# Kernel tuning notes

Measured on AMD Instinct MI355X. Metric: run time of the kernel, lower is better.

## Reference

```python
import jax, jax.numpy as jnp
import numpy as np

LOG1000 = 6.9077542789816375  # ln(1000)


def setup_inputs() -> dict:
    key = jax.random.key(0)
    kx, kp = jax.random.split(key)
    x = jax.random.normal(kx, (65536, 128), dtype=jnp.float32)
    points = jax.random.normal(kp, (2048, 128), dtype=jnp.float32)
    beta_raw = jnp.array([-3.5], dtype=jnp.float32)
    return {"x": x, "points": points, "beta_raw": beta_raw}


def reference(x, points, beta_raw):
    t1 = jnp.sum(x * x, axis=-1, keepdims=True)            # [N, 1]
    t2 = jnp.sum(points * points, axis=-1)[None, :]        # [1, P]
    t3 = 2.0 * jnp.einsum('nd,pd->np', x, points)          # [N, P]
    d2 = jnp.clip(t1 + t2 - t3, 0.0)
    min_d = jnp.min(d2, axis=-1)                           # [N]
    # translated sigmoid
    beta = jax.nn.softplus(beta_raw)                       # [1]
    alpha = -beta * LOG1000
    return jax.nn.sigmoid((min_d + alpha) / beta)
```

## Files before the change

### kernel.cpp

```cpp
#include <hip/hip_runtime.h>


#define NROWS 65536
#define NPTS  2048
#define DIMS  128
#define LOG1000F 6.9077542789816375f
#define RPB 256
#define PPB 512
#define TPB (PPB / 16)

typedef __attribute__((ext_vector_type(8))) int i32x8;
typedef __attribute__((ext_vector_type(4))) float f32x4;

union AFrag { int d[8]; i32x8 v; };
union BFrag { uint4 u4[2]; i32x8 v; };

__global__ __launch_bounds__(256) void prep_points_kernel(
    const float* __restrict__ pts, unsigned char* __restrict__ ptsf8,
    float* __restrict__ pnorm, unsigned int* __restrict__ minws)
{
    int tid  = threadIdx.x;
    int gid  = blockIdx.x * 256 + tid;
    if (gid < NROWS) minws[gid] = 0x7F800000u;

    int lane = tid & 63;
    int w    = tid >> 6;
    int pt   = blockIdx.x * 4 + w;
    const float2 v = *reinterpret_cast<const float2*>(
        pts + (size_t)pt * DIMS + lane * 2);
    int pk = __builtin_amdgcn_cvt_pk_fp8_f32(v.x, v.y, 0, false);
    *reinterpret_cast<unsigned short*>(ptsf8 + (size_t)pt * DIMS + lane * 2) =
        (unsigned short)(pk & 0xFFFF);
    float ss = v.x * v.x + v.y * v.y;
    ss += __shfl_xor(ss, 1, 64);
    ss += __shfl_xor(ss, 2, 64);
    ss += __shfl_xor(ss, 4, 64);
    ss += __shfl_xor(ss, 8, 64);
    ss += __shfl_xor(ss, 16, 64);
    ss += __shfl_xor(ss, 32, 64);
    if (lane == 0) pnorm[pt] = ss;
}

__global__ __launch_bounds__(256, 2) void distnet_main_kernel(
    const float* __restrict__ x, const unsigned char* __restrict__ ptsf8,
    const float* __restrict__ pnorm, unsigned int* __restrict__ minws)
{
    __shared__ uint4 s_b[PPB * DIMS / 16];
    __shared__ float s_pn[PPB];
    __shared__ float s_xn[RPB];

    int tid  = threadIdx.x;
    int wave = tid >> 6;
    int lane = tid & 63;
    int m    = lane & 15;
    int q    = lane >> 4;
    int rg   = blockIdx.x >> 2;
    int ph   = blockIdx.x & 3;
    int r0   = rg * RPB;
    int p0   = ph * PPB;

    const unsigned char* gbase = ptsf8;
#pragma unroll
    for (int i = 0; i < 16; ++i) {
        int tt = wave * 8 + (i >> 1);
        int c  = i & 1;
        size_t pbyte = (size_t)(p0 + tt * 16 + m) * DIMS
                       + (size_t)q * 32 + (size_t)c * 16;
        const void* g = gbase + pbyte;
        void* l = (void*)&s_b[(tt * 2 + c) * 64];
        __builtin_amdgcn_global_load_lds(
            (const __attribute__((address_space(1))) unsigned int*)g,
            (__attribute__((address_space(3))) unsigned int*)l,
            16, 0, 0);
    }
    {
        float2 v = reinterpret_cast<const float2*>(pnorm + p0)[tid];
        reinterpret_cast<float2*>(s_pn)[tid] = v;
    }

    AFrag afrag[4];
#pragma unroll
    for (int t = 0; t < 4; ++t) {
        const float* xp = x + (size_t)(r0 + wave * 64 + t * 16 + m) * DIMS
                          + q * 32;
        float ss = 0.f;
#pragma unroll
        for (int d = 0; d < 8; ++d) {
            float4 v = *reinterpret_cast<const float4*>(xp + d * 4);
            int w0 = __builtin_amdgcn_cvt_pk_fp8_f32(v.x, v.y, 0, false);
            w0 = __builtin_amdgcn_cvt_pk_fp8_f32(v.z, v.w, w0, true);
            afrag[t].d[d] = w0;
            ss += v.x * v.x + v.y * v.y + v.z * v.z + v.w * v.w;
        }
        ss += __shfl_xor(ss, 16, 64);
        ss += __shfl_xor(ss, 32, 64);
        if (lane < 16) s_xn[wave * 64 + t * 16 + lane] = ss;
    }

    __builtin_amdgcn_s_waitcnt(0x0070);
    __syncthreads();

    float runmin[4][4];
#pragma unroll
    for (int t = 0; t < 4; ++t)
#pragma unroll
        for (int r = 0; r < 4; ++r) runmin[t][r] = 1e30f;

#pragma unroll 2
    for (int tt = 0; tt < TPB; ++tt) {
        BFrag bf;
        bf.u4[0] = s_b[(tt * 2 + 0) * 64 + lane];
        bf.u4[1] = s_b[(tt * 2 + 1) * 64 + lane];
        float pn = s_pn[tt * 16 + m];
#pragma unroll
        for (int t = 0; t < 4; ++t) {
            f32x4 acc = {0.f, 0.f, 0.f, 0.f};
            acc = __builtin_amdgcn_mfma_scale_f32_16x16x128_f8f6f4(
                afrag[t].v, bf.v, acc, 0, 0, 0,
                0x7F7F7F7F, 0, 0x7F7F7F7F);
#pragma unroll
            for (int r = 0; r < 4; ++r)
                runmin[t][r] = fminf(runmin[t][r], fmaf(-2.f, acc[r], pn));
        }
    }

#pragma unroll
    for (int t = 0; t < 4; ++t) {
#pragma unroll
        for (int r = 0; r < 4; ++r) {
            float v = runmin[t][r];
            v = fminf(v, __shfl_xor(v, 1, 64));
            v = fminf(v, __shfl_xor(v, 2, 64));
            v = fminf(v, __shfl_xor(v, 4, 64));
            v = fminf(v, __shfl_xor(v, 8, 64));
            if (m == 0) {
                int rl  = wave * 64 + t * 16 + q * 4 + r;
                float d2 = fmaxf(s_xn[rl] + v, 0.f);
                atomicMin(&minws[r0 + rl], __float_as_uint(d2));
            }
        }
    }
}

__global__ __launch_bounds__(256) void finish_kernel(
    const unsigned int* __restrict__ minws,
    const float* __restrict__ beta_raw, float* __restrict__ out)
{
    int i = blockIdx.x * 256 + threadIdx.x;
    float d2    = __uint_as_float(minws[i]);
    float br    = beta_raw[0];
    float beta  = log1pf(expf(br));
    float alpha = -beta * LOG1000F;
    float z = (d2 + alpha) / beta;
    out[i] = 1.f / (1.f + expf(-z));
}

extern "C" void kernel_launch(void* const* d_in, const int* in_sizes, int n_in,
                              void* d_out, int out_size, void* d_ws, size_t ws_size,
                              hipStream_t stream) {
    const float* x        = (const float*)d_in[0];
    const float* pts      = (const float*)d_in[1];
    const float* beta_raw = (const float*)d_in[2];
    float* out            = (float*)d_out;

    unsigned char* ptsf8 = (unsigned char*)d_ws;
    float* pnorm = (float*)((char*)d_ws + (size_t)NPTS * DIMS);
    unsigned int* minws =
        (unsigned int*)((char*)d_ws + (size_t)NPTS * DIMS + NPTS * 4);

    prep_points_kernel<<<NPTS / 4, 256, 0, stream>>>(pts, ptsf8, pnorm, minws);
    distnet_main_kernel<<<(NROWS / RPB) * (NPTS / PPB), 256, 0, stream>>>(
        x, ptsf8, pnorm, minws);
    finish_kernel<<<NROWS / 256, 256, 0, stream>>>(minws, beta_raw, out);
}
```

Baseline: 112.4 us.

## Precompute fp8 x and row norms in a separate prep kernel

Adds a prep kernel that converts x to fp8 and computes row norms once, so the main kernel loads compact fp8 fragments instead of re-reading and converting fp32 x in each of the four point-phase blocks. This cuts redundant fp32 traffic and conversion work in the main kernel. In exchange it adds a kernel launch, a workspace write and read of the fp8 copy, and needs a larger workspace.

```diff
diff --git a/kernel.cpp b/kernel.cpp
--- a/kernel.cpp
+++ b/kernel.cpp
@@ -12,17 +12,40 @@
 typedef __attribute__((ext_vector_type(8))) int i32x8;
 typedef __attribute__((ext_vector_type(4))) float f32x4;
 
-union AFrag { int d[8]; i32x8 v; };
+union AFrag { uint4 u4[2]; i32x8 v; };
 union BFrag { uint4 u4[2]; i32x8 v; };
 
-__global__ __launch_bounds__(256) void prep_points_kernel(
-    const float* __restrict__ pts, unsigned char* __restrict__ ptsf8,
-    float* __restrict__ pnorm, unsigned int* __restrict__ minws)
+__global__ __launch_bounds__(256) void prep_x_kernel(
+    const float* __restrict__ x, unsigned char* __restrict__ xf8,
+    float* __restrict__ xnorm, unsigned int* __restrict__ minws)
 {
     int tid  = threadIdx.x;
     int gid  = blockIdx.x * 256 + tid;
     if (gid < NROWS) minws[gid] = 0x7F800000u;
 
+    int lane = tid & 63;
+    int w    = tid >> 6;
+    int row  = blockIdx.x * 4 + w;
+    const float2 v = *reinterpret_cast<const float2*>(
+        x + (size_t)row * DIMS + lane * 2);
+    int pk = __builtin_amdgcn_cvt_pk_fp8_f32(v.x, v.y, 0, false);
+    *reinterpret_cast<unsigned short*>(xf8 + (size_t)row * DIMS + lane * 2) =
+        (unsigned short)(pk & 0xFFFF);
+    float ss = v.x * v.x + v.y * v.y;
+    ss += __shfl_xor(ss, 1, 64);
+    ss += __shfl_xor(ss, 2, 64);
+    ss += __shfl_xor(ss, 4, 64);
+    ss += __shfl_xor(ss, 8, 64);
+    ss += __shfl_xor(ss, 16, 64);
+    ss += __shfl_xor(ss, 32, 64);
+    if (lane == 0) xnorm[row] = ss;
+}
+
+__global__ __launch_bounds__(256) void prep_points_kernel(
+    const float* __restrict__ pts, unsigned char* __restrict__ ptsf8,
+    float* __restrict__ pnorm)
+{
+    int tid  = threadIdx.x;
     int lane = tid & 63;
     int w    = tid >> 6;
     int pt   = blockIdx.x * 4 + w;
@@ -42,8 +65,9 @@
 }
 
 __global__ __launch_bounds__(256, 2) void distnet_main_kernel(
-    const float* __restrict__ x, const unsigned char* __restrict__ ptsf8,
-    const float* __restrict__ pnorm, unsigned int* __restrict__ minws)
+    const unsigned char* __restrict__ xf8, const unsigned char* __restrict__ ptsf8,
+    const float* __restrict__ pnorm, const float* __restrict__ xnorm,
+    unsigned int* __restrict__ minws)
 {
     __shared__ uint4 s_b[PPB * DIMS / 16];
     __shared__ float s_pn[PPB];
@@ -76,25 +100,16 @@
     {
         float2 v = reinterpret_cast<const float2*>(pnorm + p0)[tid];
         reinterpret_cast<float2*>(s_pn)[tid] = v;
+        s_xn[tid] = xnorm[r0 + tid];
     }
 
     AFrag afrag[4];
 #pragma unroll
     for (int t = 0; t < 4; ++t) {
-        const float* xp = x + (size_t)(r0 + wave * 64 + t * 16 + m) * DIMS
-                          + q * 32;
-        float ss = 0.f;
-#pragma unroll
-        for (int d = 0; d < 8; ++d) {
-            float4 v = *reinterpret_cast<const float4*>(xp + d * 4);
-            int w0 = __builtin_amdgcn_cvt_pk_fp8_f32(v.x, v.y, 0, false);
-            w0 = __builtin_amdgcn_cvt_pk_fp8_f32(v.z, v.w, w0, true);
-            afrag[t].d[d] = w0;
-            ss += v.x * v.x + v.y * v.y + v.z * v.z + v.w * v.w;
-        }
-        ss += __shfl_xor(ss, 16, 64);
-        ss += __shfl_xor(ss, 32, 64);
-        if (lane < 16) s_xn[wave * 64 + t * 16 + lane] = ss;
+        const uint4* xp = reinterpret_cast<const uint4*>(
+            xf8 + (size_t)(r0 + wave * 64 + t * 16 + m) * DIMS + q * 32);
+        afrag[t].u4[0] = xp[0];
+        afrag[t].u4[1] = xp[1];
     }
 
     __builtin_amdgcn_s_waitcnt(0x0070);
@@ -163,13 +178,16 @@
     const float* beta_raw = (const float*)d_in[2];
     float* out            = (float*)d_out;
 
-    unsigned char* ptsf8 = (unsigned char*)d_ws;
-    float* pnorm = (float*)((char*)d_ws + (size_t)NPTS * DIMS);
-    unsigned int* minws =
-        (unsigned int*)((char*)d_ws + (size_t)NPTS * DIMS + NPTS * 4);
+    char* ws = (char*)d_ws;
+    unsigned char* ptsf8 = (unsigned char*)ws;
+    float* pnorm  = (float*)(ws + 256 * 1024);
+    unsigned int* minws = (unsigned int*)(ws + 264 * 1024);
+    unsigned char* xf8  = (unsigned char*)(ws + 520 * 1024);
+    float* xnorm  = (float*)(ws + 520 * 1024 + (size_t)NROWS * DIMS);
 
-    prep_points_kernel<<<NPTS / 4, 256, 0, stream>>>(pts, ptsf8, pnorm, minws);
+    prep_x_kernel<<<NROWS / 4, 256, 0, stream>>>(x, xf8, xnorm, minws);
+    prep_points_kernel<<<NPTS / 4, 256, 0, stream>>>(pts, ptsf8, pnorm);
     distnet_main_kernel<<<(NROWS / RPB) * (NPTS / PPB), 256, 0, stream>>>(
-        x, ptsf8, pnorm, minws);
+        xf8, ptsf8, pnorm, xnorm, minws);
     finish_kernel<<<NROWS / 256, 256, 0, stream>>>(minws, beta_raw, out);
 }
```

Result: faster. 109.0 us (-3.0%).
